# Optimization experiments

Measured on AMD Instinct MI355X. Metric: run time of the kernel, lower is better.

The kernel has to match this reference:

```python
import jax, jax.numpy as jnp
import numpy as np

GX, GY = 480, 360          # BEV grid (grid_size[0], grid_size[1])
C_OUT = 32                 # fea_compre
MAX_PT = 256               # max_pt_per_encode
NUM_VOX = GX * GY
BN_EPS = 1e-5


def setup_inputs() -> dict:
    key = jax.random.key(0)
    ks = jax.random.split(key, 12)
    B, N, F = 2, 100000, 7
    pt_fea = jax.random.normal(ks[0], (B, N, F), jnp.float32)
    xy_ind = jnp.stack([
        jax.random.randint(ks[1], (B, N), 0, GX),
        jax.random.randint(ks[2], (B, N), 0, GY),
    ], axis=-1).astype(jnp.int32)

    def lin(k, i, o):
        return 0.02 * jax.random.normal(k, (o, i), jnp.float32)

    inp = {"pt_fea": pt_fea, "xy_ind": xy_ind}
    dims = [(F, 64), (64, 128), (128, 256), (256, 512)]
    for j, (i, o) in enumerate(dims):
        inp[f"w{j}"] = lin(ks[3 + j], i, o)
        inp[f"b{j}"] = jnp.zeros((o,), jnp.float32)
    # BatchNorm (eval mode): bn0 on raw features, bn1..bn3 after linears 0..2
    for j, d in enumerate([F, 64, 128, 256]):
        inp[f"g{j}"] = jnp.ones((d,), jnp.float32)
        inp[f"be{j}"] = jnp.zeros((d,), jnp.float32)
        inp[f"m{j}"] = jnp.zeros((d,), jnp.float32)
        inp[f"v{j}"] = jnp.ones((d,), jnp.float32)
    inp["wc"] = lin(ks[7], 512, C_OUT)
    inp["bc"] = jnp.zeros((C_OUT,), jnp.float32)
    return inp


def _bn(x, g, b, m, v):
    return (x - m) * (g * jax.lax.rsqrt(v + BN_EPS)) + b


def reference(pt_fea, xy_ind,
              w0, b0, w1, b1, w2, b2, w3, b3,
              g0, be0, m0, v0, g1, be1, m1, v1,
              g2, be2, m2, v2, g3, be3, m3, v3,
              wc, bc):
    def pointnet(x):  # [N, 7] -> [N, 512]
        x = _bn(x, g0, be0, m0, v0)
        x = jax.nn.relu(_bn(x @ w0.T + b0, g1, be1, m1, v1))
        x = jax.nn.relu(_bn(x @ w1.T + b1, g2, be2, m2, v2))
        x = jax.nn.relu(_bn(x @ w2.T + b2, g3, be3, m3, v3))
        return x @ w3.T + b3

    def one_cloud(fea, xy):  # fea [N,7], xy [N,2] int
        N = fea.shape[0]
        vox = xy[:, 0] * GY + xy[:, 1]                      # linear voxel id
        # rank of each point within its voxel group (== grp_range_torch output)
        order = jnp.argsort(vox, stable=True)
        sid = vox[order]
        new_grp = jnp.concatenate([jnp.array([True]), sid[1:] != sid[:-1]])
        start = jax.lax.cummax(jnp.where(new_grp, jnp.arange(N), 0))
        rank_sorted = jnp.arange(N) - start
        rank = jnp.zeros((N,), rank_sorted.dtype).at[order].set(rank_sorted)
        remain = rank < MAX_PT                              # cap points per voxel

        pn = pointnet(fea)                                  # [N, 512]
        seg = jnp.where(remain, vox, NUM_VOX)               # dropped pts -> dummy seg
        maxf = jax.ops.segment_max(pn, seg, num_segments=NUM_VOX + 1)[:NUM_VOX]
        cnt = jax.ops.segment_sum(jnp.ones((N,), jnp.int32), seg,
                                  num_segments=NUM_VOX + 1)[:NUM_VOX]
        occ = (cnt > 0)[:, None]
        maxf = jnp.where(occ, maxf, 0.0)                    # kill -inf of empty voxels
        comp = jnp.where(occ, jax.nn.relu(maxf @ wc.T + bc), 0.0)  # [NUM_VOX, 32]
        return comp.reshape(GX, GY, C_OUT)

    grid = jax.vmap(one_cloud)(pt_fea, xy_ind)              # [B, GX, GY, 32]
    return jnp.transpose(grid, (0, 3, 1, 2))                # [B, 32, GX, GY]
```

## Files before the change

kernel.cpp:

```cpp
#include <hip/hip_runtime.h>

#define DEV __device__ __forceinline__

typedef _Float16 f16;
typedef __attribute__((ext_vector_type(8))) _Float16 half8;
typedef __attribute__((ext_vector_type(4))) _Float16 half4;
typedef __attribute__((ext_vector_type(4))) float floatx4;

constexpr int GXc = 480, GYc = 360;
constexpr int NVOX = GXc * GYc;
constexpr int BATCH = 2;
constexpr int NPT = 100000;
constexpr int FIN = 7;
constexpr int COUT = 32;
constexpr int MAXPT = 256;
constexpr float EPS = 1e-5f;
constexpr int NBLK = (NVOX + 255) / 256;
constexpr int FSTRIDE = NPT + 2;
constexpr int NB_PTS = (BATCH * NPT + 255) / 256;
constexpr int NB_FL  = (NPT + 255) / 256;

DEV unsigned f2ord(float f) {
  unsigned b = __float_as_uint(f);
  return (b & 0x80000000u) ? ~b : (b | 0x80000000u);
}
DEV float ord2f(unsigned u) {
  return __uint_as_float((u & 0x80000000u) ? (u & 0x7FFFFFFFu) : ~u);
}

__global__ __launch_bounds__(256)
void k_foldcount(const float* __restrict__ w0, const float* __restrict__ b0,
                 const float* __restrict__ w1, const float* __restrict__ b1,
                 const float* __restrict__ w2, const float* __restrict__ b2,
                 const float* __restrict__ w3, const float* __restrict__ wc,
                 const float* __restrict__ g0, const float* __restrict__ be0, const float* __restrict__ m0, const float* __restrict__ v0,
                 const float* __restrict__ g1, const float* __restrict__ be1, const float* __restrict__ m1, const float* __restrict__ v1,
                 const float* __restrict__ g2, const float* __restrict__ be2, const float* __restrict__ m2, const float* __restrict__ v2,
                 const float* __restrict__ g3, const float* __restrict__ be3, const float* __restrict__ m3, const float* __restrict__ v3,
                 float* __restrict__ A0, float* __restrict__ c0,
                 f16* __restrict__ A1h, float* __restrict__ c1,
                 f16* __restrict__ A2h, float* __restrict__ c2,
                 f16* __restrict__ W3h, f16* __restrict__ Wch,
                 const int* __restrict__ xy, int* __restrict__ vox, int* __restrict__ cnt)
{
  int blk = blockIdx.x;
  if (blk < 512) {
    int id = blk * 256 + threadIdx.x;
    if (id < 131072) W3h[id] = (f16)w3[id];
    if (id < 32768) { int m = id >> 7; A2h[id] = (f16)(w2[id] * (g3[m] * rsqrtf(v3[m] + EPS))); }
    if (id < 16384) Wch[id] = (f16)wc[id];
    if (id < 8192)  { int m = id >> 6; A1h[id] = (f16)(w1[id] * (g2[m] * rsqrtf(v2[m] + EPS))); }
    if (id < 512) {
      int m = id >> 3, k = id & 7;
      A0[id] = (k < 7) ? w0[m * 7 + k] * (g0[k] * rsqrtf(v0[k] + EPS)) * (g1[m] * rsqrtf(v1[m] + EPS)) : 0.f;
    }
    if (id < 64) {
      float t1m = g1[id] * rsqrtf(v1[id] + EPS);
      float a = b0[id];
      for (int k = 0; k < 7; k++) {
        float t0k = g0[k] * rsqrtf(v0[k] + EPS);
        a += (be0[k] - m0[k] * t0k) * w0[id * 7 + k];
      }
      c0[id] = (a - m1[id]) * t1m + be1[id];
    }
    if (id < 128) c1[id] = (b1[id] - m2[id]) * (g2[id] * rsqrtf(v2[id] + EPS)) + be2[id];
    if (id < 256) c2[id] = (b2[id] - m3[id]) * (g3[id] * rsqrtf(v3[id] + EPS)) + be3[id];
  } else {
    int id = (blk - 512) * 256 + threadIdx.x;
    if (id >= BATCH * NPT) return;
    int b = id / NPT;
    int x = xy[id * 2 + 0], y = xy[id * 2 + 1];
    int v = x * GYc + y;
    vox[id] = v;
    atomicAdd(&cnt[b * NVOX + v], 1);
  }
}

__global__ __launch_bounds__(256)
void k_scan1(const int* __restrict__ cnt, int* __restrict__ slot, int* __restrict__ pofs,
             unsigned long long* __restrict__ bsum)
{
  __shared__ unsigned long long sc[256];
  int g = blockIdx.x, tid = threadIdx.x;
  int b = g / NBLK, blk = g % NBLK;
  int v = blk * 256 + tid;
  int c = (v < NVOX) ? cnt[b * NVOX + v] : 0;
  unsigned long long val = ((unsigned long long)(c > 0 ? 1u : 0u) << 32) | (unsigned)c;
  sc[tid] = val;
  __syncthreads();
  for (int off = 1; off < 256; off <<= 1) {
    unsigned long long t = (tid >= off) ? sc[tid - off] : 0ull;
    __syncthreads();
    sc[tid] += t;
    __syncthreads();
  }
  if (v < NVOX) {
    unsigned long long e = sc[tid] - val;
    slot[b * NVOX + v] = (int)(e >> 32);
    pofs[b * NVOX + v] = (int)(unsigned)e;
  }
  if (tid == 255) bsum[g] = sc[255];
}

__global__ __launch_bounds__(256)
void k_scan2(const unsigned long long* __restrict__ bsum, unsigned long long* __restrict__ boff,
             int* __restrict__ Stot)
{
  __shared__ unsigned long long sc[256];
  int b = blockIdx.x, tid = threadIdx.x;
  unsigned long long run = 0;
  for (int i0 = 0; i0 < NBLK; i0 += 256) {
    int i = i0 + tid;
    unsigned long long val = (i < NBLK) ? bsum[b * NBLK + i] : 0ull;
    sc[tid] = val;
    __syncthreads();
    for (int off = 1; off < 256; off <<= 1) {
      unsigned long long t = (tid >= off) ? sc[tid - off] : 0ull;
      __syncthreads();
      sc[tid] += t;
      __syncthreads();
    }
    if (i < NBLK) boff[b * NBLK + i] = run + sc[tid] - val;
    run += sc[255];
    __syncthreads();
  }
  if (tid == 0) Stot[b] = (int)(run >> 32);
}

__global__ __launch_bounds__(256)
void k_scan3(const int* __restrict__ cnt, int* __restrict__ slot, int* __restrict__ pofs,
             const unsigned long long* __restrict__ boff, int* __restrict__ occv,
             int* __restrict__ flag)
{
  int g = blockIdx.x, tid = threadIdx.x;
  int b = g / NBLK, blk = g % NBLK;
  int v = blk * 256 + tid;
  if (v >= NVOX) return;
  unsigned long long bo = boff[g];
  int s = slot[b * NVOX + v] + (int)(bo >> 32);
  int pp = pofs[b * NVOX + v] + (int)(unsigned)bo;
  slot[b * NVOX + v] = s;
  pofs[b * NVOX + v] = pp;
  int c = cnt[b * NVOX + v];
  if (c > 0) {
    occv[b * NPT + s] = v;
    int use = (c > MAXPT) ? MAXPT : c;
    bool capped = (c > MAXPT);
    bool span = ((pp >> 2) != ((pp + use - 1) >> 2));
    if (span || capped) atomicOr(&flag[b * FSTRIDE + s], 1);
    if (capped) atomicOr(&flag[b * FSTRIDE + s + 1], 1);
  }
}

__global__ __launch_bounds__(256)
void k_postscan(const int* __restrict__ vox, const int* __restrict__ pofs,
                const int* __restrict__ slot, int* __restrict__ tmp,
                int* __restrict__ order, int* __restrict__ sgrp,
                const int* __restrict__ flag, const int* __restrict__ Stot,
                int* __restrict__ nflag, int* __restrict__ flaglist)
{
  int blk = blockIdx.x;
  if (blk < NB_PTS) {
    int id = blk * 256 + threadIdx.x;
    if (id >= BATCH * NPT) return;
    int b = id / NPT, p = id - b * NPT;
    int v = vox[id];
    int r = atomicAdd(&tmp[b * NVOX + v], 1);
    int pos = pofs[b * NVOX + v] + r;
    order[b * NPT + pos] = p;
    sgrp[b * NPT + pos] = (r < MAXPT) ? slot[b * NVOX + v] : -2;
  } else {
    int rb = blk - NB_PTS;
    int b = rb / NB_FL;
    int s = (rb % NB_FL) * 256 + threadIdx.x;
    if (s >= Stot[b]) return;
    if (flag[b * FSTRIDE + s]) {
      int i = atomicAdd(&nflag[b], 1);
      flaglist[b * NPT + i] = s;
    }
  }
}

__global__ __launch_bounds__(256)
void k_zero_flagged(unsigned* __restrict__ maxf, const int* __restrict__ flaglist,
                    const int* __restrict__ nflag, int b, int scap)
{
  long long n = (long long)nflag[b] * 128;
  uint4 z; z.x = z.y = z.z = z.w = 0u;
  long long stride = (long long)gridDim.x * 256;
  for (long long i = (long long)blockIdx.x * 256 + threadIdx.x; i < n; i += stride) {
    int s = flaglist[b * NPT + (int)(i >> 7)];
    if (s < scap) ((uint4*)(maxf + (size_t)s * 512))[i & 127] = z;
  }
}

__global__ __launch_bounds__(256)
void k_mlp012(const float* __restrict__ X, const int* __restrict__ order,
              const float* __restrict__ A0, const float* __restrict__ c0,
              const f16* __restrict__ A1h, const float* __restrict__ c1,
              const f16* __restrict__ A2h, const float* __restrict__ c2,
              f16* __restrict__ H3, int P)
{
  __shared__ __align__(16) char smem[65536];
  f16* H2s = (f16*)smem;
  f16* H1s = (f16*)(smem + 32768);
  f16* W1s = (f16*)(smem + 49152);
  float* A0s = (float*)smem;
  float* c0s = A0s + 512;
  f16* W2s = (f16*)(smem + 32768);

  const int tid = threadIdx.x;
  const int p0 = blockIdx.x * 128;
  const int wv = tid >> 6, ln = tid & 63;
  const int wp = (wv & 1) * 64, wm = (wv >> 1) * 64;
  const int l15 = ln & 15, lq = ln >> 4;

  A0s[tid] = A0[tid];
  A0s[tid + 256] = A0[tid + 256];
  if (tid < 64) c0s[tid] = c0[tid];
  #pragma unroll
  for (int it = 0; it < 4; it++) {
    int idx = it * 256 + tid;
    int r = idx >> 3, q = idx & 7;
    *(half8*)&W1s[r * 64 + (q ^ (r & 7)) * 8] = *(const half8*)(A1h + r * 64 + q * 8);
  }
  __syncthreads();

  {
    int p = tid >> 1, h = tid & 1;
    int pos = p0 + p; if (pos > P - 1) pos = P - 1;
    int pt = order[pos];
    float f[7];
    #pragma unroll
    for (int k = 0; k < 7; k++) f[k] = X[(size_t)pt * 7 + k];
    #pragma unroll
    for (int mm4 = 0; mm4 < 8; mm4++) {
      int mb = h * 32 + mm4 * 4;
      half4 ov;
      #pragma unroll
      for (int j = 0; j < 4; j++) {
        int m = mb + j;
        float a = c0s[m];
        #pragma unroll
        for (int k = 0; k < 7; k++) a += f[k] * A0s[m * 8 + k];
        ov[j] = (f16)(a > 0.f ? a : 0.f);
      }
      *(half4*)&H1s[p * 64 + ((mb >> 3) ^ (p & 7)) * 8 + (mb & 7)] = ov;
    }
  }
  __syncthreads();

  {
    floatx4 acc[4][4];
    #pragma unroll
    for (int i = 0; i < 4; i++)
      #pragma unroll
      for (int j = 0; j < 4; j++) acc[i][j] = (floatx4)0.f;
    #pragma unroll
    for (int k0 = 0; k0 < 64; k0 += 32) {
      half8 af[4], bf[4];
      #pragma unroll
      for (int i = 0; i < 4; i++) {
        int row = wp + i * 16 + l15;
        af[i] = *(const half8*)&H1s[row * 64 + (((k0 >> 3) + lq) ^ (row & 7)) * 8];
      }
      #pragma unroll
      for (int j = 0; j < 4; j++) {
        int row = wm + j * 16 + l15;
        bf[j] = *(const half8*)&W1s[row * 64 + (((k0 >> 3) + lq) ^ (row & 7)) * 8];
      }
      #pragma unroll
      for (int i = 0; i < 4; i++)
        #pragma unroll
        for (int j = 0; j < 4; j++)
          acc[i][j] = __builtin_amdgcn_mfma_f32_16x16x32_f16(af[i], bf[j], acc[i][j], 0, 0, 0);
    }
    float c1j[4];
    #pragma unroll
    for (int j = 0; j < 4; j++) c1j[j] = c1[wm + j * 16 + l15];
    #pragma unroll
    for (int i = 0; i < 4; i++) {
      #pragma unroll
      for (int r = 0; r < 4; r++) {
        int row = wp + i * 16 + lq * 4 + r;
        #pragma unroll
        for (int j = 0; j < 4; j++) {
          int col = wm + j * 16 + l15;
          float v = acc[i][j][r] + c1j[j];
          if (v < 0.f) v = 0.f;
          H2s[row * 128 + ((col >> 3) ^ (row & 7)) * 8 + (col & 7)] = (f16)v;
        }
      }
    }
  }
  __syncthreads();

  for (int mc = 0; mc < 2; mc++) {
    floatx4 acc[4][4];
    #pragma unroll
    for (int i = 0; i < 4; i++)
      #pragma unroll
      for (int j = 0; j < 4; j++) acc[i][j] = (floatx4)0.f;
    for (int k0 = 0; k0 < 128; k0 += 32) {
      __syncthreads();
      #pragma unroll
      for (int it = 0; it < 2; it++) {
        int idx = it * 256 + tid;
        int r = idx >> 2, q = idx & 3;
        *(half8*)&W2s[r * 40 + q * 8] =
            *(const half8*)(A2h + (size_t)(mc * 128 + r) * 128 + k0 + q * 8);
      }
      __syncthreads();
      half8 af[4], bf[4];
      #pragma unroll
      for (int i = 0; i < 4; i++) {
        int row = wp + i * 16 + l15;
        af[i] = *(const half8*)&H2s[row * 128 + (((k0 >> 3) + lq) ^ (row & 7)) * 8];
      }
      #pragma unroll
      for (int j = 0; j < 4; j++)
        bf[j] = *(const half8*)&W2s[(wm + j * 16 + l15) * 40 + lq * 8];
      #pragma unroll
      for (int i = 0; i < 4; i++)
        #pragma unroll
        for (int j = 0; j < 4; j++)
          acc[i][j] = __builtin_amdgcn_mfma_f32_16x16x32_f16(af[i], bf[j], acc[i][j], 0, 0, 0);
    }
    float c2j[4];
    #pragma unroll
    for (int j = 0; j < 4; j++) c2j[j] = c2[mc * 128 + wm + j * 16 + l15];
    #pragma unroll
    for (int i = 0; i < 4; i++) {
      #pragma unroll
      for (int r = 0; r < 4; r++) {
        int prow = p0 + wp + i * 16 + lq * 4 + r;
        if (prow < P) {
          #pragma unroll
          for (int j = 0; j < 4; j++) {
            int col = mc * 128 + wm + j * 16 + l15;
            float v = acc[i][j][r] + c2j[j];
            if (v < 0.f) v = 0.f;
            H3[(size_t)prow * 256 + col] = (f16)v;
          }
        }
      }
    }
  }
}

constexpr int LW = 40;

__global__ __launch_bounds__(256)
void k_gemm16_smax(const f16* __restrict__ A, const f16* __restrict__ W,
                   const float* __restrict__ bias, int P,
                   unsigned* __restrict__ maxf, const int* __restrict__ sg,
                   int chunk0, int rest, int scap, int nxpad)
{
  constexpr int K = 256, M = 512;
  __shared__ f16 Xs[128 * LW];
  __shared__ f16 Ws[128 * LW];
  const int tid = threadIdx.x;
  const int xb = blockIdx.x % nxpad;
  const int yb = blockIdx.x / nxpad;
  if (xb * 128 >= P) return;
  const int p0 = xb * 128;
  const int m0 = yb * 128;
  const int wv = tid >> 6, ln = tid & 63;
  const int wp = (wv & 1) * 64, wm = (wv >> 1) * 64;
  const int l15 = ln & 15, lq = ln >> 4;

  floatx4 acc[4][4];
  #pragma unroll
  for (int i = 0; i < 4; i++)
    #pragma unroll
    for (int j = 0; j < 4; j++) acc[i][j] = (floatx4)0.f;

  const int sr = tid >> 2, sq = tid & 3;
  for (int k0 = 0; k0 < K; k0 += 32) {
    {
      int pr = p0 + sr; if (pr > P - 1) pr = P - 1;
      *(half8*)&Xs[sr * LW + sq * 8] = *(const half8*)(A + (size_t)pr * K + k0 + sq * 8);
      *(half8*)&Ws[sr * LW + sq * 8] = *(const half8*)(W + (size_t)(m0 + sr) * K + k0 + sq * 8);
      int r2 = sr + 64;
      int pr2 = p0 + r2; if (pr2 > P - 1) pr2 = P - 1;
      *(half8*)&Xs[r2 * LW + sq * 8] = *(const half8*)(A + (size_t)pr2 * K + k0 + sq * 8);
      *(half8*)&Ws[r2 * LW + sq * 8] = *(const half8*)(W + (size_t)(m0 + r2) * K + k0 + sq * 8);
    }
    __syncthreads();
    half8 af[4], bf[4];
    #pragma unroll
    for (int i = 0; i < 4; i++)
      af[i] = *(const half8*)&Xs[(wp + i * 16 + l15) * LW + lq * 8];
    #pragma unroll
    for (int j = 0; j < 4; j++)
      bf[j] = *(const half8*)&Ws[(wm + j * 16 + l15) * LW + lq * 8];
    #pragma unroll
    for (int i = 0; i < 4; i++)
      #pragma unroll
      for (int j = 0; j < 4; j++)
        acc[i][j] = __builtin_amdgcn_mfma_f32_16x16x32_f16(af[i], bf[j], acc[i][j], 0, 0, 0);
    __syncthreads();
  }

  float bj[4];
  #pragma unroll
  for (int j = 0; j < 4; j++) bj[j] = bias[m0 + wm + j * 16 + l15];
  const int cbase = m0 + wm + l15;

  #pragma unroll
  for (int i = 0; i < 4; i++) {
    int pr0 = p0 + wp + i * 16 + lq * 4;
    float run[4];
    int gcur = -1;
    bool openL = false;

    auto flushrun = [&](int gc, bool open) {
      if (gc >= scap) return;
      unsigned* row = maxf + (size_t)gc * M + cbase;
      if (open) {
        #pragma unroll
        for (int j = 0; j < 4; j++) atomicMax(row + j * 16, f2ord(run[j]));
      } else {
        #pragma unroll
        for (int j = 0; j < 4; j++) row[j * 16] = f2ord(run[j]);
      }
    };

    int glast = (chunk0 + pr0 > 0) ? sg[pr0 - 1] : -1;
    #pragma unroll
    for (int r = 0; r < 4; r++) {
      int pos = pr0 + r;
      int g = (pos < P) ? sg[pos] : -1;
      if (g >= 0) {
        if (g == gcur) {
          #pragma unroll
          for (int j = 0; j < 4; j++) run[j] = fmaxf(run[j], acc[i][j][r] + bj[j]);
        } else {
          if (gcur >= 0) flushrun(gcur, openL);
          gcur = g;
          openL = (glast == g) || (glast == -2);
          #pragma unroll
          for (int j = 0; j < 4; j++) run[j] = acc[i][j][r] + bj[j];
        }
      } else {
        if (gcur >= 0) { flushrun(gcur, openL || (g == -2)); gcur = -1; }
      }
      glast = g;
    }
    if (gcur >= 0) {
      int gnext = (pr0 + 4 < rest) ? sg[pr0 + 4] : -1;
      flushrun(gcur, openL || (gnext == gcur) || (gnext == -2));
    }
  }
}

__global__ __launch_bounds__(256)
void k_compress_mfma(const unsigned* __restrict__ maxf, const f16* __restrict__ Wch,
                     const float* __restrict__ bc, const int* __restrict__ Stot,
                     float* __restrict__ outc, int scap)
{
  int S = Stot[0]; if (S > scap) S = scap;
  const int s0 = blockIdx.x * 128;
  if (s0 >= S) return;
  __shared__ f16 Xs[128 * LW];
  __shared__ f16 Wcs[32 * LW];
  const int tid = threadIdx.x;
  const int wv = tid >> 6, ln = tid & 63;
  const int l15 = ln & 15, lq = ln >> 4;

  floatx4 acc[2][2];
  #pragma unroll
  for (int i = 0; i < 2; i++)
    #pragma unroll
    for (int j = 0; j < 2; j++) acc[i][j] = (floatx4)0.f;

  for (int k0 = 0; k0 < 512; k0 += 32) {
    #pragma unroll
    for (int l = 0; l < 4; l++) {
      int idx = l * 256 + tid;
      int r = idx >> 3, q = idx & 7;
      int srow = s0 + r; if (srow > S - 1) srow = S - 1;
      uint4 uv = *(const uint4*)(maxf + (size_t)srow * 512 + k0 + q * 4);
      half4 hv;
      hv[0] = (f16)ord2f(uv.x); hv[1] = (f16)ord2f(uv.y);
      hv[2] = (f16)ord2f(uv.z); hv[3] = (f16)ord2f(uv.w);
      *(half4*)&Xs[r * LW + q * 4] = hv;
    }
    {
      int c = tid >> 3, q = tid & 7;
      *(half4*)&Wcs[c * LW + q * 4] = *(const half4*)(Wch + (size_t)c * 512 + k0 + q * 4);
    }
    __syncthreads();
    half8 af[2], bf[2];
    #pragma unroll
    for (int i = 0; i < 2; i++)
      af[i] = *(const half8*)&Xs[(wv * 32 + i * 16 + l15) * LW + lq * 8];
    #pragma unroll
    for (int j = 0; j < 2; j++)
      bf[j] = *(const half8*)&Wcs[(j * 16 + l15) * LW + lq * 8];
    #pragma unroll
    for (int i = 0; i < 2; i++)
      #pragma unroll
      for (int j = 0; j < 2; j++)
        acc[i][j] = __builtin_amdgcn_mfma_f32_16x16x32_f16(af[i], bf[j], acc[i][j], 0, 0, 0);
    __syncthreads();
  }

  #pragma unroll
  for (int i = 0; i < 2; i++) {
    int sb = s0 + wv * 32 + i * 16 + lq * 4;
    #pragma unroll
    for (int r = 0; r < 4; r++) {
      int s = sb + r;
      if (s < S) {
        #pragma unroll
        for (int j = 0; j < 2; j++) {
          int c = j * 16 + l15;
          float v = acc[i][j][r] + bc[c];
          outc[(size_t)s * COUT + c] = v > 0.f ? v : 0.f;
        }
      }
    }
  }
}

__global__ __launch_bounds__(256)
void k_scatter_out(const float* __restrict__ outc, const int* __restrict__ cnt,
                   const int* __restrict__ slot, float* __restrict__ outb, int scap)
{
  int v = blockIdx.x * 256 + threadIdx.x;
  if (v >= NVOX) return;
  bool occ = cnt[v] > 0;
  int s = slot[v];
  float4 a[8];
  if (occ && s < scap) {
    #pragma unroll
    for (int q = 0; q < 8; q++) a[q] = *(const float4*)(outc + (size_t)s * COUT + q * 4);
  } else {
    #pragma unroll
    for (int q = 0; q < 8; q++) { a[q].x = 0.f; a[q].y = 0.f; a[q].z = 0.f; a[q].w = 0.f; }
  }
  const float* af = (const float*)a;
  #pragma unroll
  for (int c = 0; c < 32; c++) outb[(size_t)c * NVOX + v] = af[c];
}

extern "C" void kernel_launch(void* const* d_in, const int* in_sizes, int n_in,
                              void* d_out, int out_size, void* d_ws, size_t ws_size,
                              hipStream_t stream) {
  (void)in_sizes; (void)n_in; (void)out_size;
  const float* pt_fea = (const float*)d_in[0];
  const int*   xy     = (const int*)d_in[1];
  const float* w0 = (const float*)d_in[2];  const float* b0 = (const float*)d_in[3];
  const float* w1 = (const float*)d_in[4];  const float* b1 = (const float*)d_in[5];
  const float* w2 = (const float*)d_in[6];  const float* b2 = (const float*)d_in[7];
  const float* w3 = (const float*)d_in[8];  const float* b3 = (const float*)d_in[9];
  const float* g0 = (const float*)d_in[10]; const float* be0 = (const float*)d_in[11];
  const float* m0 = (const float*)d_in[12]; const float* v0  = (const float*)d_in[13];
  const float* g1 = (const float*)d_in[14]; const float* be1 = (const float*)d_in[15];
  const float* m1 = (const float*)d_in[16]; const float* v1  = (const float*)d_in[17];
  const float* g2 = (const float*)d_in[18]; const float* be2 = (const float*)d_in[19];
  const float* m2 = (const float*)d_in[20]; const float* v2  = (const float*)d_in[21];
  const float* g3 = (const float*)d_in[22]; const float* be3 = (const float*)d_in[23];
  const float* m3 = (const float*)d_in[24]; const float* v3  = (const float*)d_in[25];
  const float* wc = (const float*)d_in[26]; const float* bc = (const float*)d_in[27];
  float* outp = (float*)d_out;

  char* base = (char*)d_ws;
  size_t off = 0;
  auto alloc = [&](size_t n) -> void* {
    void* p = base + off;
    off = (off + n + 255) & ~(size_t)255;
    return p;
  };
  float* A0f = (float*)alloc(512 * 4);    float* c0f = (float*)alloc(64 * 4);
  f16* A1h = (f16*)alloc(8192 * 2);       float* c1f = (float*)alloc(128 * 4);
  f16* A2h = (f16*)alloc(32768 * 2);      float* c2f = (float*)alloc(256 * 4);
  f16* W3h = (f16*)alloc(131072 * 2);
  f16* Wch = (f16*)alloc(16384 * 2);
  int* vox  = (int*)alloc((size_t)BATCH * NPT * 4);
  int* slot = (int*)alloc((size_t)BATCH * NVOX * 4);
  int* pofs = (int*)alloc((size_t)BATCH * NVOX * 4);
  unsigned long long* bsum = (unsigned long long*)alloc((size_t)BATCH * NBLK * 8);
  unsigned long long* boff = (unsigned long long*)alloc((size_t)BATCH * NBLK * 8);
  int* Stot = (int*)alloc((size_t)BATCH * 4);
  int* occv = (int*)alloc((size_t)BATCH * NPT * 4);
  int* order = (int*)alloc((size_t)BATCH * NPT * 4);
  int* sgrp  = (int*)alloc((size_t)BATCH * NPT * 4);
  int* flist = (int*)alloc((size_t)BATCH * NPT * 4);
  float* outc = (float*)alloc((size_t)NPT * COUT * 4);
  size_t zoff0 = off;
  int* cnt  = (int*)alloc((size_t)BATCH * NVOX * 4);
  int* tmp  = (int*)alloc((size_t)BATCH * NVOX * 4);
  int* flag = (int*)alloc((size_t)BATCH * FSTRIDE * 4);
  int* nflag = (int*)alloc((size_t)BATCH * 4);
  size_t zlen = off - zoff0;

  int scap = NPT;
  size_t remain = (ws_size > off) ? ws_size - off : 0;
  size_t minH = (size_t)128 * 256 * 2;
  if (remain < (size_t)scap * 512 * 4 + minH) {
    size_t avail = (remain > minH) ? remain - minH : 0;
    scap = (int)(avail / 2048);
    if (scap < 1) scap = 1;
  }
  unsigned* maxf = (unsigned*)alloc((size_t)scap * 512 * 4);

  size_t hrem = (ws_size > off) ? ws_size - off : 0;
  int P = (int)((hrem / ((size_t)256 * 2)) & ~(size_t)127);
  if (P > NPT) P = ((NPT + 127) / 128) * 128;
  if (P < 128) P = 128;
  f16* H3 = (f16*)alloc((size_t)P * 256 * 2);

  hipMemsetAsync(base + zoff0, 0, zlen, stream);

  k_foldcount<<<512 + NB_PTS, 256, 0, stream>>>(w0, b0, w1, b1, w2, b2, w3, wc,
                                                g0, be0, m0, v0, g1, be1, m1, v1,
                                                g2, be2, m2, v2, g3, be3, m3, v3,
                                                A0f, c0f, A1h, c1f, A2h, c2f, W3h, Wch,
                                                xy, vox, cnt);
  k_scan1<<<BATCH * NBLK, 256, 0, stream>>>(cnt, slot, pofs, bsum);
  k_scan2<<<BATCH, 256, 0, stream>>>(bsum, boff, Stot);
  k_scan3<<<BATCH * NBLK, 256, 0, stream>>>(cnt, slot, pofs, boff, occv, flag);
  k_postscan<<<NB_PTS + BATCH * NB_FL, 256, 0, stream>>>(vox, pofs, slot, tmp, order, sgrp,
                                                         flag, Stot, nflag, flist);

  for (int b = 0; b < BATCH; b++) {
    k_zero_flagged<<<128, 256, 0, stream>>>(maxf, flist, nflag, b, scap);
    for (int p0 = 0; p0 < NPT; p0 += P) {
      int pc = (NPT - p0 < P) ? (NPT - p0) : P;
      k_mlp012<<<(pc + 127) / 128, 256, 0, stream>>>(pt_fea + (size_t)b * NPT * FIN,
                                                     order + (size_t)b * NPT + p0,
                                                     A0f, c0f, A1h, c1f, A2h, c2f,
                                                     H3, pc);
      int nxb = (pc + 127) / 128;
      int nxpad = (nxb + 7) & ~7;
      k_gemm16_smax<<<nxpad * 4, 256, 0, stream>>>(H3, W3h, b3, pc,
                                                   maxf, sgrp + (size_t)b * NPT + p0,
                                                   p0, NPT - p0, scap, nxpad);
    }
    k_compress_mfma<<<(NPT + 127) / 128, 256, 0, stream>>>(maxf, Wch, bc, Stot + b,
                                                           outc, scap);
    k_scatter_out<<<(NVOX + 255) / 256, 256, 0, stream>>>(outc, cnt + (size_t)b * NVOX,
                                                          slot + (size_t)b * NVOX,
                                                          outp + (size_t)b * COUT * NVOX,
                                                          scap);
  }
}
```

Measured before the change: 565.6 us.

## Fold flagged-row zeroing into MLP launch and register-prefetch GEMM tiles

Removes the separate k_zero_flagged launch by appending extra zeroing blocks to the first k_mlp012 grid of each batch, so zeroing runs alongside the MLP. The layer-3 GEMM now prefetches the next K-slice of A and W into registers before the barrier, overlapping global loads with MFMA work. The compress kernel loads all of Wc into LDS once with an XOR swizzle and register-prefetches the maxf tiles. The trade-offs are higher register and LDS use per block, which may lower occupancy.

Measured after the change: 529.8 us. -6.3%, faster.

```diff
diff --git a/kernel.cpp b/kernel.cpp
--- a/kernel.cpp
+++ b/kernel.cpp
@@ -19,6 +19,7 @@
 constexpr int FSTRIDE = NPT + 2;
 constexpr int NB_PTS = (BATCH * NPT + 255) / 256;
 constexpr int NB_FL  = (NPT + 255) / 256;
+constexpr int ZB = 128;
 
 DEV unsigned f2ord(float f) {
   unsigned b = __float_as_uint(f);
@@ -182,25 +183,26 @@
 }
 
 __global__ __launch_bounds__(256)
-void k_zero_flagged(unsigned* __restrict__ maxf, const int* __restrict__ flaglist,
-                    const int* __restrict__ nflag, int b, int scap)
-{
-  long long n = (long long)nflag[b] * 128;
-  uint4 z; z.x = z.y = z.z = z.w = 0u;
-  long long stride = (long long)gridDim.x * 256;
-  for (long long i = (long long)blockIdx.x * 256 + threadIdx.x; i < n; i += stride) {
-    int s = flaglist[b * NPT + (int)(i >> 7)];
-    if (s < scap) ((uint4*)(maxf + (size_t)s * 512))[i & 127] = z;
-  }
-}
-
-__global__ __launch_bounds__(256)
 void k_mlp012(const float* __restrict__ X, const int* __restrict__ order,
               const float* __restrict__ A0, const float* __restrict__ c0,
               const f16* __restrict__ A1h, const float* __restrict__ c1,
               const f16* __restrict__ A2h, const float* __restrict__ c2,
-              f16* __restrict__ H3, int P)
-{
+              f16* __restrict__ H3, int P, int nmlp,
+              unsigned* __restrict__ maxf, const int* __restrict__ flaglist,
+              const int* __restrict__ nflag, int b, int scap)
+{
+  if (blockIdx.x >= nmlp) {
+    int zb = blockIdx.x - nmlp;
+    long long n = (long long)nflag[b] * 128;
+    uint4 z; z.x = z.y = z.z = z.w = 0u;
+    long long stride = (long long)ZB * 256;
+    for (long long i = (long long)zb * 256 + threadIdx.x; i < n; i += stride) {
+      int s = flaglist[b * NPT + (int)(i >> 7)];
+      if (s < scap) ((uint4*)(maxf + (size_t)s * 512))[i & 127] = z;
+    }
+    return;
+  }
+
   __shared__ __align__(16) char smem[65536];
   f16* H2s = (f16*)smem;
   f16* H1s = (f16*)(smem + 32768);
@@ -376,15 +378,29 @@
     for (int j = 0; j < 4; j++) acc[i][j] = (floatx4)0.f;
 
   const int sr = tid >> 2, sq = tid & 3;
+  int pr = p0 + sr;      if (pr > P - 1) pr = P - 1;
+  int pr2 = p0 + sr + 64; if (pr2 > P - 1) pr2 = P - 1;
+  const f16* aptr0 = A + (size_t)pr * K + sq * 8;
+  const f16* aptr1 = A + (size_t)pr2 * K + sq * 8;
+  const f16* wptr0 = W + (size_t)(m0 + sr) * K + sq * 8;
+  const f16* wptr1 = W + (size_t)(m0 + sr + 64) * K + sq * 8;
+
+  half8 ra0 = *(const half8*)(aptr0);
+  half8 ra1 = *(const half8*)(aptr1);
+  half8 rw0 = *(const half8*)(wptr0);
+  half8 rw1 = *(const half8*)(wptr1);
+
+  #pragma unroll
   for (int k0 = 0; k0 < K; k0 += 32) {
-    {
-      int pr = p0 + sr; if (pr > P - 1) pr = P - 1;
-      *(half8*)&Xs[sr * LW + sq * 8] = *(const half8*)(A + (size_t)pr * K + k0 + sq * 8);
-      *(half8*)&Ws[sr * LW + sq * 8] = *(const half8*)(W + (size_t)(m0 + sr) * K + k0 + sq * 8);
-      int r2 = sr + 64;
-      int pr2 = p0 + r2; if (pr2 > P - 1) pr2 = P - 1;
-      *(half8*)&Xs[r2 * LW + sq * 8] = *(const half8*)(A + (size_t)pr2 * K + k0 + sq * 8);
-      *(half8*)&Ws[r2 * LW + sq * 8] = *(const half8*)(W + (size_t)(m0 + r2) * K + k0 + sq * 8);
+    *(half8*)&Xs[sr * LW + sq * 8]        = ra0;
+    *(half8*)&Xs[(sr + 64) * LW + sq * 8] = ra1;
+    *(half8*)&Ws[sr * LW + sq * 8]        = rw0;
+    *(half8*)&Ws[(sr + 64) * LW + sq * 8] = rw1;
+    if (k0 + 32 < K) {
+      ra0 = *(const half8*)(aptr0 + k0 + 32);
+      ra1 = *(const half8*)(aptr1 + k0 + 32);
+      rw0 = *(const half8*)(wptr0 + k0 + 32);
+      rw1 = *(const half8*)(wptr1 + k0 + 32);
     }
     __syncthreads();
     half8 af[4], bf[4];
@@ -462,42 +478,66 @@
   int S = Stot[0]; if (S > scap) S = scap;
   const int s0 = blockIdx.x * 128;
   if (s0 >= S) return;
+  __shared__ f16 Wcs[32 * 512];
   __shared__ f16 Xs[128 * LW];
-  __shared__ f16 Wcs[32 * LW];
   const int tid = threadIdx.x;
   const int wv = tid >> 6, ln = tid & 63;
   const int l15 = ln & 15, lq = ln >> 4;
 
+  #pragma unroll
+  for (int it = 0; it < 8; it++) {
+    int idx = it * 256 + tid;
+    int row = idx >> 6, oct = idx & 63;
+    *(half8*)&Wcs[row * 512 + (oct >> 3) * 64 + ((oct & 7) ^ (row & 7)) * 8] =
+        *(const half8*)(Wch + (size_t)row * 512 + oct * 8);
+  }
+
+  const unsigned* aq[4];
+  #pragma unroll
+  for (int l = 0; l < 4; l++) {
+    int idx = l * 256 + tid;
+    int r = idx >> 3, q = idx & 7;
+    int srow = s0 + r; if (srow > S - 1) srow = S - 1;
+    aq[l] = maxf + (size_t)srow * 512 + q * 4;
+  }
+
   floatx4 acc[2][2];
   #pragma unroll
   for (int i = 0; i < 2; i++)
     #pragma unroll
     for (int j = 0; j < 2; j++) acc[i][j] = (floatx4)0.f;
 
+  uint4 pf[4];
+  #pragma unroll
+  for (int l = 0; l < 4; l++) pf[l] = *(const uint4*)(aq[l]);
+
+  #pragma unroll
   for (int k0 = 0; k0 < 512; k0 += 32) {
     #pragma unroll
     for (int l = 0; l < 4; l++) {
       int idx = l * 256 + tid;
       int r = idx >> 3, q = idx & 7;
-      int srow = s0 + r; if (srow > S - 1) srow = S - 1;
-      uint4 uv = *(const uint4*)(maxf + (size_t)srow * 512 + k0 + q * 4);
       half4 hv;
-      hv[0] = (f16)ord2f(uv.x); hv[1] = (f16)ord2f(uv.y);
-      hv[2] = (f16)ord2f(uv.z); hv[3] = (f16)ord2f(uv.w);
+      hv[0] = (f16)ord2f(pf[l].x); hv[1] = (f16)ord2f(pf[l].y);
+      hv[2] = (f16)ord2f(pf[l].z); hv[3] = (f16)ord2f(pf[l].w);
       *(half4*)&Xs[r * LW + q * 4] = hv;
     }
-    {
-      int c = tid >> 3, q = tid & 7;
-      *(half4*)&Wcs[c * LW + q * 4] = *(const half4*)(Wch + (size_t)c * 512 + k0 + q * 4);
+    if (k0 + 32 < 512) {
+      #pragma unroll
+      for (int l = 0; l < 4; l++) pf[l] = *(const uint4*)(aq[l] + k0 + 32);
     }
     __syncthreads();
     half8 af[2], bf[2];
     #pragma unroll
     for (int i = 0; i < 2; i++)
       af[i] = *(const half8*)&Xs[(wv * 32 + i * 16 + l15) * LW + lq * 8];
-    #pragma unroll
-    for (int j = 0; j < 2; j++)
-      bf[j] = *(const half8*)&Wcs[(j * 16 + l15) * LW + lq * 8];
+    int oct = (k0 >> 3) + lq;
+    int hi64 = (oct >> 3) * 64, lo = oct & 7;
+    #pragma unroll
+    for (int j = 0; j < 2; j++) {
+      int row = j * 16 + l15;
+      bf[j] = *(const half8*)&Wcs[row * 512 + hi64 + (lo ^ (row & 7)) * 8];
+    }
     #pragma unroll
     for (int i = 0; i < 2; i++)
       #pragma unroll
@@ -626,15 +666,16 @@
                                                          flag, Stot, nflag, flist);
 
   for (int b = 0; b < BATCH; b++) {
-    k_zero_flagged<<<128, 256, 0, stream>>>(maxf, flist, nflag, b, scap);
     for (int p0 = 0; p0 < NPT; p0 += P) {
       int pc = (NPT - p0 < P) ? (NPT - p0) : P;
-      k_mlp012<<<(pc + 127) / 128, 256, 0, stream>>>(pt_fea + (size_t)b * NPT * FIN,
-                                                     order + (size_t)b * NPT + p0,
-                                                     A0f, c0f, A1h, c1f, A2h, c2f,
-                                                     H3, pc);
-      int nxb = (pc + 127) / 128;
-      int nxpad = (nxb + 7) & ~7;
+      int nmlp = (pc + 127) / 128;
+      int gext = (p0 == 0) ? ZB : 0;
+      k_mlp012<<<nmlp + gext, 256, 0, stream>>>(pt_fea + (size_t)b * NPT * FIN,
+                                                order + (size_t)b * NPT + p0,
+                                                A0f, c0f, A1h, c1f, A2h, c2f,
+                                                H3, pc, nmlp,
+                                                maxf, flist, nflag, b, scap);
+      int nxpad = (nmlp + 7) & ~7;
       k_gemm16_smax<<<nxpad * 4, 256, 0, stream>>>(H3, W3h, b3, pc,
                                                    maxf, sgrp + (size_t)b * NPT + p0,
                                                    p0, NPT - p0, scap, nxpad);
```
